# Optimization experiments

Hardware: AMD Instinct MI355X
Metric: run time of the kernel (lower is better)

Reference implementation:

```python
import jax, jax.numpy as jnp
import numpy as np

L_MODES = 64
GRID = 128
OUT_GRID = 128
CIN = 64
COUT = 64
T_DIM = 256


def legendre_table(L, theta):
    """Fully-normalized associated Legendre P_bar_l^m(cos(theta)), Condon-Shortley.
    Returns (L, 2L-1, n_theta) with m indexed -(L-1)..(L-1) at axis 1."""
    nt = theta.shape[0]
    x = np.cos(theta)
    s = np.sin(theta)
    P = np.zeros((L, L, nt))
    P[0, 0] = np.sqrt(1.0 / (4.0 * np.pi))
    for m in range(1, L):
        P[m, m] = -np.sqrt((2.0 * m + 1.0) / (2.0 * m)) * s * P[m - 1, m - 1]
    for m in range(L - 1):
        P[m + 1, m] = np.sqrt(2.0 * m + 3.0) * x * P[m, m]
    for m in range(L):
        for l in range(m + 2, L):
            a = np.sqrt((4.0 * l * l - 1.0) / (l * l - m * m))
            b = np.sqrt(((l - 1.0) ** 2 - m * m) / (4.0 * (l - 1.0) ** 2 - 1.0))
            P[l, m] = a * (x * P[l - 1, m] - b * P[l - 2, m])
    T = np.zeros((L, 2 * L - 1, nt))
    for m in range(L):
        T[:, L - 1 + m, :] = P[:, m, :]
        if m > 0:
            T[:, L - 1 - m, :] = ((-1.0) ** m) * P[:, m, :]
    return T.astype(np.float32)


def setup_inputs() -> dict:
    key = jax.random.key(0)
    ks = jax.random.split(key, 8)
    theta = np.pi * (np.arange(GRID) + 0.5) / GRID
    theta_out = np.pi * (np.arange(OUT_GRID) + 0.5) / OUT_GRID
    P_in = jnp.asarray(legendre_table(L_MODES, theta))            # (L, 2L-1, GRID)
    P_out = jnp.asarray(legendre_table(L_MODES, theta_out))       # (L, 2L-1, OUT_GRID)
    quad_w = jnp.asarray((np.pi / GRID) * np.sin(theta), dtype=jnp.float32)
    scale_w = 1.0 / (CIN + COUT)
    return {
        "x": jax.random.normal(ks[0], (GRID, GRID, CIN), jnp.float32),
        "t_emb": jax.random.normal(ks[1], (T_DIM,), jnp.float32),
        "wr": scale_w * jax.random.normal(ks[2], (L_MODES, 2 * L_MODES - 1, CIN, COUT), jnp.float32),
        "wi": scale_w * jax.random.normal(ks[3], (L_MODES, 2 * L_MODES - 1, CIN, COUT), jnp.float32),
        "conv_w": jax.random.normal(ks[4], (CIN, COUT), jnp.float32) / np.sqrt(CIN),
        "conv_b": jnp.zeros((COUT,), jnp.float32),
        "time_w": jax.random.normal(ks[5], (COUT, COUT), jnp.float32),
        "dense_w": jax.random.normal(ks[6], (T_DIM, 2 * COUT), jnp.float32) / np.sqrt(T_DIM),
        "ln_scale": jnp.ones((COUT,), jnp.float32),
        "ln_bias": jnp.zeros((COUT,), jnp.float32),
        "P_in": P_in,
        "P_out": P_out,
        "quad_w": quad_w,
    }


def reference(x, t_emb, wr, wi, conv_w, conv_b, time_w, dense_w, ln_scale, ln_bias, P_in, P_out, quad_w):
    L = P_in.shape[0]
    G_out = P_out.shape[2]
    nlon = x.shape[1]
    m_idx = np.arange(-(L - 1), L)

    # ---- forward spherical harmonic transform (lon FFT + Legendre quadrature) ----
    f = jnp.fft.fft(x.astype(jnp.complex64), axis=1) * (2.0 * np.pi / nlon)  # (nlat, nlon, Cin)
    fm = f[:, np.mod(m_idx, nlon), :] * quad_w[:, None, None]                # (nlat, 2L-1, Cin)
    flm = jnp.einsum('tmc,lmt->lmc', fm, P_in)                                # (L, 2L-1, Cin)

    # ---- per-(l,m) complex spectral conv ----
    w = wr + 1j * wi
    flm = jnp.einsum('lmi,lmio->lmo', flm, w)                                 # (L, 2L-1, Cout)

    # ---- inverse SHT onto output grid ----
    g = jnp.einsum('lmo,lmt->tmo', flm, P_out)                                # (G_out, 2L-1, Cout)
    phi = 2.0 * np.pi * np.arange(G_out) / G_out
    E = jnp.asarray(np.exp(1j * np.outer(m_idx, phi)).astype(np.complex64))   # (2L-1, G_out)
    x_spec = jnp.real(jnp.einsum('tmo,mk->tko', g, E))                        # (G_out, G_out, Cout)

    # ---- residual time-conditioned path (TimeConv2D, einsum as written in source) ----
    h = jnp.einsum('lmk,ko->lmo', x, conv_w) + conv_b                          # 1x1 conv
    psi = t_emb @ dense_w
    w_t, b_t = jnp.split(psi, 2, axis=-1)
    h = jnp.einsum('ij,j,lmk->lmi', time_w, w_t, h) + b_t[None, None, :]
    h = jax.image.resize(h, (G_out, G_out, h.shape[-1]), method='bicubic')

    # ---- add, layernorm over channels, relu ----
    out = x_spec + h
    mu = jnp.mean(out, axis=-1, keepdims=True)
    var = jnp.var(out, axis=-1, keepdims=True)
    out = (out - mu) * jax.lax.rsqrt(var + 1e-6) * ln_scale + ln_bias
    return jax.nn.relu(out)
```

## Files before the change

kernel.cpp:

```cpp
#include <hip/hip_runtime.h>
#include <math.h>

#define LM 64
#define MM 127
#define GG 128
#define CC 64
#define OO 64

#define TWO_PI 6.28318530717958647692f

__global__ __launch_bounds__(256) void k_dft(const float* __restrict__ x,
                                             const float* __restrict__ quad_w,
                                             const float* __restrict__ conv_w,
                                             const float* __restrict__ conv_b,
                                             const float* __restrict__ t_emb,
                                             const float* __restrict__ dense_w,
                                             const float* __restrict__ time_w,
                                             float2* __restrict__ F,
                                             float* __restrict__ Sv,
                                             float* __restrict__ aux) {
    int b = blockIdx.x;
    int tx = threadIdx.x;

    if (b == 256) {
        __shared__ float psis[128];
        if (tx < 128) {
            float acc = 0.f;
            for (int tq = 0; tq < 256; ++tq) acc += t_emb[tq] * dense_w[tq * 128 + tx];
            psis[tx] = acc;
            aux[tx] = acc;
        }
        __syncthreads();
        if (tx < 64) {
            float tv = 0.f;
            for (int q = 0; q < 64; ++q) tv += time_w[tx * 64 + q] * psis[q];
            aux[128 + tx] = tv;
        }
        return;
    }

    int t = b >> 1, ch = b & 1;
    int c0base = ch * 32;

    __shared__ __align__(16) float xs[GG * 32];
    __shared__ float2 tab[GG];
    __shared__ float cwsl[32];
    __shared__ float Sp[2][GG];
    __shared__ float bsum_s;

    {
        const float* xp = x + (size_t)t * GG * CC + c0base;
        for (int idx = tx; idx < GG * 32 / 4; idx += 256) {
            int n = idx >> 3, cq = idx & 7;
            *(float4*)&xs[n * 32 + cq * 4] = *(const float4*)&xp[n * CC + cq * 4];
        }
    }
    if (tx < GG) {
        float ang = (TWO_PI / GG) * tx;
        tab[tx] = make_float2(cosf(ang), sinf(ang));
    }
    if (tx >= 128 && tx < 160) {
        int c = c0base + (tx - 128);
        float s = 0.f;
        for (int o = 0; o < OO; ++o) s += conv_w[c * OO + o];
        cwsl[tx - 128] = s;
    }
    if (tx == 160) {
        float bs = 0.f;
        for (int o = 0; o < OO; ++o) bs += conv_b[o];
        bsum_s = bs;
    }
    __syncthreads();

    int k = tx & 63, cgl = tx >> 6;
    int c0 = cgl * 8;

    float sr[8], si[8];
#pragma unroll
    for (int j = 0; j < 8; ++j) { sr[j] = 0.f; si[j] = 0.f; }

    int kn = 0;
    for (int n = 0; n < GG; ++n) {
        float2 w = tab[kn];
        const float4 v0 = *(const float4*)&xs[n * 32 + c0];
        const float4 v1 = *(const float4*)&xs[n * 32 + c0 + 4];
        float vv[8] = {v0.x, v0.y, v0.z, v0.w, v1.x, v1.y, v1.z, v1.w};
#pragma unroll
        for (int j = 0; j < 8; ++j) {
            sr[j] += vv[j] * w.x;
            si[j] -= vv[j] * w.y;
        }
        kn = (kn + k) & (GG - 1);
    }
    float sc = (TWO_PI / GG) * quad_w[t];

    {
        float2* Fp = F + ((size_t)t * 64 + k) * CC + c0base + c0;
#pragma unroll
        for (int q = 0; q < 4; ++q) {
            float4 v = make_float4(sr[2 * q] * sc, si[2 * q] * sc,
                                   sr[2 * q + 1] * sc, si[2 * q + 1] * sc);
            *(float4*)&Fp[2 * q] = v;
        }
    }

    {
        int n2 = tx & 127, h = tx >> 7;
        float p = 0.f;
#pragma unroll
        for (int j = 0; j < 16; ++j) p += xs[n2 * 32 + h * 16 + j] * cwsl[h * 16 + j];
        Sp[h][n2] = p;
    }
    __syncthreads();
    if (tx < GG) {
        float v = Sp[0][tx] + Sp[1][tx] + (ch == 0 ? bsum_s : 0.f);
        Sv[(size_t)ch * GG * GG + t * GG + tx] = v;
    }
}

__global__ __launch_bounds__(256) void k_leg_fwd(const float2* __restrict__ F,
                                                 const float* __restrict__ P_in,
                                                 float2* __restrict__ flm) {
    int m = blockIdx.x;
    int lh = blockIdx.y;
    int l0 = lh * 32;
    if (l0 + 31 < m) return;

    __shared__ __align__(16) float2 Fs[64 * 64];
    __shared__ __align__(16) float  Ps[128 * 36];
    int tx = threadIdx.x;
    int c = tx & 63, lg = tx >> 6;

    for (int idx = tx; idx < 32 * 128; idx += 256) {
        int lr = idx >> 7, t = idx & 127;
        Ps[t * 36 + lr] = P_in[((size_t)(l0 + lr) * MM + 63 + m) * GG + t];
    }

    float sr[8], si[8];
#pragma unroll
    for (int j = 0; j < 8; ++j) { sr[j] = 0.f; si[j] = 0.f; }

    for (int tp = 0; tp < 2; ++tp) {
        __syncthreads();
        for (int idx = tx; idx < 64 * 64; idx += 256) {
            int tl = idx >> 6, cc = idx & 63;
            Fs[idx] = F[((size_t)(tp * 64 + tl) * 64 + m) * CC + cc];
        }
        __syncthreads();
        for (int tl = 0; tl < 64; ++tl) {
            int t = tp * 64 + tl;
            float2 f = Fs[tl * 64 + c];
            const float* pp = &Ps[t * 36 + lg * 8];
            float4 p0 = *(const float4*)pp;
            float4 p1 = *(const float4*)(pp + 4);
            float pv[8] = {p0.x, p0.y, p0.z, p0.w, p1.x, p1.y, p1.z, p1.w};
#pragma unroll
            for (int j = 0; j < 8; ++j) {
                sr[j] += f.x * pv[j];
                si[j] += f.y * pv[j];
            }
        }
    }
#pragma unroll
    for (int j = 0; j < 8; ++j) {
        int l = l0 + lg * 8 + j;
        if (l >= m) flm[((size_t)l * 64 + m) * CC + c] = make_float2(sr[j], si[j]);
    }
}

__global__ __launch_bounds__(256) void k_wmul(const float2* __restrict__ flm,
                                              const float* __restrict__ wr,
                                              const float* __restrict__ wi,
                                              float2* __restrict__ flm2) {
    int l = blockIdx.x, mi = blockIdx.y;
    int m = mi - 63;
    int am = m < 0 ? -m : m;
    if (l < am) return;
    __shared__ float2 fs[CC];
    __shared__ float2 part[16][CC];
    int tx = threadIdx.x, ol = tx & 15, ig = tx >> 4;
    if (tx < 64) {
        float2 f = flm[((size_t)l * 64 + am) * CC + tx];
        if (m < 0) {
            float sgn = (am & 1) ? -1.f : 1.f;
            f.x *= sgn;
            f.y *= -sgn;
        }
        fs[tx] = f;
    }
    __syncthreads();
    size_t base = ((size_t)(l * MM + mi) * CC) * OO;
    const float4* wr4 = (const float4*)(wr + base);
    const float4* wi4 = (const float4*)(wi + base);
    float ar[4] = {0.f, 0.f, 0.f, 0.f}, ai[4] = {0.f, 0.f, 0.f, 0.f};
#pragma unroll
    for (int di = 0; di < 4; ++di) {
        int i = ig * 4 + di;
        float4 a = wr4[i * 16 + ol];
        float4 b = wi4[i * 16 + ol];
        float2 f = fs[i];
        ar[0] += f.x * a.x - f.y * b.x;  ai[0] += f.x * b.x + f.y * a.x;
        ar[1] += f.x * a.y - f.y * b.y;  ai[1] += f.x * b.y + f.y * a.y;
        ar[2] += f.x * a.z - f.y * b.z;  ai[2] += f.x * b.z + f.y * a.z;
        ar[3] += f.x * a.w - f.y * b.w;  ai[3] += f.x * b.w + f.y * a.w;
    }
#pragma unroll
    for (int j = 0; j < 4; ++j) part[ig][ol * 4 + j] = make_float2(ar[j], ai[j]);
    __syncthreads();
    if (tx < 64) {
        float rr = 0.f, ri = 0.f;
#pragma unroll
        for (int q = 0; q < 16; ++q) {
            float2 p = part[q][tx];
            rr += p.x;
            ri += p.y;
        }
        flm2[(size_t)(l * MM + mi) * OO + tx] = make_float2(rr, ri);
    }
}

__global__ __launch_bounds__(256) void k_leg_inv(const float2* __restrict__ flm2,
                                                 const float* __restrict__ P_out,
                                                 float2* __restrict__ g) {
    int mi = blockIdx.x;
    int th = blockIdx.y >> 1, oh = blockIdx.y & 1;
    int t0 = th * 64, o0 = oh * 32;

    __shared__ __align__(16) float2 Ws[64 * 32];
    __shared__ __align__(16) float  Ps[64 * 64];
    int tx = threadIdx.x;
    int ol = tx & 31, tg = tx >> 5;
    int o = o0 + ol;

    for (int idx = tx; idx < 64 * 32; idx += 256) {
        int ls = idx >> 5, oo = idx & 31;
        Ws[idx] = flm2[(size_t)(ls * MM + mi) * OO + o0 + oo];
    }
    for (int idx = tx; idx < 64 * 64; idx += 256) {
        int ls = idx >> 6, tt = idx & 63;
        Ps[idx] = P_out[((size_t)ls * MM + mi) * GG + t0 + tt];
    }
    __syncthreads();

    float gr[8], gi[8];
#pragma unroll
    for (int j = 0; j < 8; ++j) { gr[j] = 0.f; gi[j] = 0.f; }

    for (int l = 0; l < 64; ++l) {
        float2 wv = Ws[l * 32 + ol];
        const float* pp = &Ps[l * 64 + tg * 8];
        float4 p0 = *(const float4*)pp;
        float4 p1 = *(const float4*)(pp + 4);
        float pv[8] = {p0.x, p0.y, p0.z, p0.w, p1.x, p1.y, p1.z, p1.w};
#pragma unroll
        for (int j = 0; j < 8; ++j) {
            gr[j] += wv.x * pv[j];
            gi[j] += wv.y * pv[j];
        }
    }
#pragma unroll
    for (int j = 0; j < 8; ++j) {
        int t = t0 + tg * 8 + j;
        g[((size_t)t * MM + mi) * OO + o] = make_float2(gr[j], gi[j]);
    }
}

__global__ __launch_bounds__(512) void k_final(const float2* __restrict__ g,
                                               const float* __restrict__ Sv,
                                               const float* __restrict__ aux,
                                               const float* __restrict__ ln_scale,
                                               const float* __restrict__ ln_bias,
                                               float* __restrict__ out) {
    __shared__ float2 gs[64 * 64];
    __shared__ float Ss[64];
    int t = blockIdx.x, kh = blockIdx.y;
    int tx = threadIdx.x;
    int o = tx & 63, kg = tx >> 6;

    if (tx < 64)
        Ss[tx] = Sv[t * GG + kh * 64 + tx] + Sv[GG * GG + t * GG + kh * 64 + tx];

    float zr[8], zi[8], accr[8], acci[8];
#pragma unroll
    for (int j = 0; j < 8; ++j) {
        int k = kh * 64 + kg * 8 + j;
        float phi = (TWO_PI / GG) * k;
        float s, c;
        __sincosf(phi, &s, &c);
        zr[j] = c; zi[j] = s;
        accr[j] = 0.f; acci[j] = 0.f;
    }

    for (int pass = 0; pass < 2; ++pass) {
        int mbase = (pass == 0) ? 64 : 0;
        int cnt = (pass == 0) ? 63 : 64;
        __syncthreads();
        for (int idx = tx; idx < cnt * 64; idx += 512) {
            int mm = idx >> 6, oo = idx & 63;
            gs[idx] = g[((size_t)t * MM + mbase + mm) * OO + oo];
        }
        __syncthreads();
        for (int mm = cnt - 1; mm >= 0; --mm) {
            float2 gv = gs[mm * 64 + o];
#pragma unroll
            for (int j = 0; j < 8; ++j) {
                float tr = accr[j] * zr[j] - acci[j] * zi[j] + gv.x;
                float ti = accr[j] * zi[j] + acci[j] * zr[j] + gv.y;
                accr[j] = tr; acci[j] = ti;
            }
        }
    }

    float tvec = aux[128 + o], bt = aux[64 + o];
    float lns = ln_scale[o], lnb = ln_bias[o];
#pragma unroll
    for (int j = 0; j < 8; ++j) {
        int k = kh * 64 + kg * 8 + j;
        float phi = (TWO_PI / GG) * k;
        float s63, c63;
        sincosf(63.f * phi, &s63, &c63);
        float xsp = accr[j] * c63 + acci[j] * s63;
        float val = xsp + tvec * Ss[k - kh * 64] + bt;

        float mu = val;
#pragma unroll
        for (int off = 1; off < 64; off <<= 1) mu += __shfl_xor(mu, off);
        mu *= (1.f / 64.f);
        float d = val - mu;
        float var = d * d;
#pragma unroll
        for (int off = 1; off < 64; off <<= 1) var += __shfl_xor(var, off);
        var *= (1.f / 64.f);
        float r = d * rsqrtf(var + 1e-6f) * lns + lnb;
        out[((size_t)(t * GG) + k) * OO + o] = fmaxf(r, 0.f);
    }
}

extern "C" void kernel_launch(void* const* d_in, const int* in_sizes, int n_in,
                              void* d_out, int out_size, void* d_ws, size_t ws_size,
                              hipStream_t stream) {
    const float* x        = (const float*)d_in[0];
    const float* t_emb    = (const float*)d_in[1];
    const float* wr       = (const float*)d_in[2];
    const float* wi       = (const float*)d_in[3];
    const float* conv_w   = (const float*)d_in[4];
    const float* conv_b   = (const float*)d_in[5];
    const float* time_w   = (const float*)d_in[6];
    const float* dense_w  = (const float*)d_in[7];
    const float* ln_scale = (const float*)d_in[8];
    const float* ln_bias  = (const float*)d_in[9];
    const float* P_in     = (const float*)d_in[10];
    const float* P_out    = (const float*)d_in[11];
    const float* quad_w   = (const float*)d_in[12];

    float* ws = (float*)d_ws;
    float*  aux  = ws;
    float2* F    = (float2*)(ws + 512);
    float2* flm  = (float2*)(ws + 1049088);
    float2* flm2 = (float2*)(ws + 1573376);
    float2* g    = (float2*)(ws + 2613760);
    float*  Sv   = ws + 4694528;

    float* out = (float*)d_out;

    k_dft<<<257, 256, 0, stream>>>(x, quad_w, conv_w, conv_b, t_emb, dense_w, time_w,
                                   F, Sv, aux);
    k_leg_fwd<<<dim3(64, 2), 256, 0, stream>>>(F, P_in, flm);
    k_wmul<<<dim3(LM, MM), 256, 0, stream>>>(flm, wr, wi, flm2);
    k_leg_inv<<<dim3(MM, 4), 256, 0, stream>>>(flm2, P_out, g);
    k_final<<<dim3(GG, 2), 512, 0, stream>>>(g, Sv, aux, ln_scale, ln_bias, out);
}
```

Measured before the change: 341.5 us.

## Split DFT, forward Legendre and inverse Legendre across more blocks for occupancy

The channel-split DFT now runs 512 blocks of 16 channels, and the forward Legendre transform is split over four theta chunks that write partial sums which k_wmul reduces. The inverse Legendre kernel uses smaller theta tiles, giving twice as many blocks. k_final replaces a per-element sincosf(63*phi) with a sign-flip identity and sums four partial S vectors. The aim is to fill more compute units on small grids, at the cost of extra partial-sum traffic and less per-thread reuse.

```diff
diff --git a/kernel.cpp b/kernel.cpp
--- a/kernel.cpp
+++ b/kernel.cpp
@@ -22,7 +22,7 @@
     int b = blockIdx.x;
     int tx = threadIdx.x;
 
-    if (b == 256) {
+    if (b == 512) {
         __shared__ float psis[128];
         if (tx < 128) {
             float acc = 0.f;
@@ -39,54 +39,54 @@
         return;
     }
 
-    int t = b >> 1, ch = b & 1;
-    int c0base = ch * 32;
-
-    __shared__ __align__(16) float xs[GG * 32];
+    int t = b >> 2, cq = b & 3;
+    int c0base = cq * 16;
+
+    __shared__ __align__(16) float xs[GG * 16];
     __shared__ float2 tab[GG];
-    __shared__ float cwsl[32];
+    __shared__ float cwsl[16];
     __shared__ float Sp[2][GG];
     __shared__ float bsum_s;
 
     {
         const float* xp = x + (size_t)t * GG * CC + c0base;
-        for (int idx = tx; idx < GG * 32 / 4; idx += 256) {
-            int n = idx >> 3, cq = idx & 7;
-            *(float4*)&xs[n * 32 + cq * 4] = *(const float4*)&xp[n * CC + cq * 4];
+        for (int idx = tx; idx < GG * 16 / 4; idx += 256) {
+            int n = idx >> 2, c4 = idx & 3;
+            *(float4*)&xs[n * 16 + c4 * 4] = *(const float4*)&xp[n * CC + c4 * 4];
         }
     }
     if (tx < GG) {
         float ang = (TWO_PI / GG) * tx;
         tab[tx] = make_float2(cosf(ang), sinf(ang));
     }
-    if (tx >= 128 && tx < 160) {
+    if (tx >= 128 && tx < 144) {
         int c = c0base + (tx - 128);
         float s = 0.f;
         for (int o = 0; o < OO; ++o) s += conv_w[c * OO + o];
         cwsl[tx - 128] = s;
     }
-    if (tx == 160) {
+    if (tx == 144) {
         float bs = 0.f;
         for (int o = 0; o < OO; ++o) bs += conv_b[o];
         bsum_s = bs;
     }
     __syncthreads();
 
-    int k = tx & 63, cgl = tx >> 6;
-    int c0 = cgl * 8;
-
-    float sr[8], si[8];
-#pragma unroll
-    for (int j = 0; j < 8; ++j) { sr[j] = 0.f; si[j] = 0.f; }
+    int k = tx & 63, cg = tx >> 6;
+    int c0 = cg * 4;
+
+    float sr[4], si[4];
+#pragma unroll
+    for (int j = 0; j < 4; ++j) { sr[j] = 0.f; si[j] = 0.f; }
 
     int kn = 0;
+#pragma unroll 4
     for (int n = 0; n < GG; ++n) {
         float2 w = tab[kn];
-        const float4 v0 = *(const float4*)&xs[n * 32 + c0];
-        const float4 v1 = *(const float4*)&xs[n * 32 + c0 + 4];
-        float vv[8] = {v0.x, v0.y, v0.z, v0.w, v1.x, v1.y, v1.z, v1.w};
-#pragma unroll
-        for (int j = 0; j < 8; ++j) {
+        const float4 v = *(const float4*)&xs[n * 16 + c0];
+        float vv[4] = {v.x, v.y, v.z, v.w};
+#pragma unroll
+        for (int j = 0; j < 4; ++j) {
             sr[j] += vv[j] * w.x;
             si[j] -= vv[j] * w.y;
         }
@@ -96,79 +96,75 @@
 
     {
         float2* Fp = F + ((size_t)t * 64 + k) * CC + c0base + c0;
-#pragma unroll
-        for (int q = 0; q < 4; ++q) {
-            float4 v = make_float4(sr[2 * q] * sc, si[2 * q] * sc,
-                                   sr[2 * q + 1] * sc, si[2 * q + 1] * sc);
-            *(float4*)&Fp[2 * q] = v;
-        }
+        *(float4*)&Fp[0] = make_float4(sr[0] * sc, si[0] * sc, sr[1] * sc, si[1] * sc);
+        *(float4*)&Fp[2] = make_float4(sr[2] * sc, si[2] * sc, sr[3] * sc, si[3] * sc);
     }
 
     {
         int n2 = tx & 127, h = tx >> 7;
         float p = 0.f;
 #pragma unroll
-        for (int j = 0; j < 16; ++j) p += xs[n2 * 32 + h * 16 + j] * cwsl[h * 16 + j];
+        for (int j = 0; j < 8; ++j) p += xs[n2 * 16 + h * 8 + j] * cwsl[h * 8 + j];
         Sp[h][n2] = p;
     }
     __syncthreads();
     if (tx < GG) {
-        float v = Sp[0][tx] + Sp[1][tx] + (ch == 0 ? bsum_s : 0.f);
-        Sv[(size_t)ch * GG * GG + t * GG + tx] = v;
+        float v = Sp[0][tx] + Sp[1][tx] + (cq == 0 ? bsum_s : 0.f);
+        Sv[(size_t)cq * GG * GG + t * GG + tx] = v;
     }
 }
 
 __global__ __launch_bounds__(256) void k_leg_fwd(const float2* __restrict__ F,
                                                  const float* __restrict__ P_in,
-                                                 float2* __restrict__ flm) {
+                                                 float2* __restrict__ flmp) {
     int m = blockIdx.x;
     int lh = blockIdx.y;
+    int tq = blockIdx.z;
     int l0 = lh * 32;
     if (l0 + 31 < m) return;
-
-    __shared__ __align__(16) float2 Fs[64 * 64];
-    __shared__ __align__(16) float  Ps[128 * 36];
+    int t0 = tq * 32;
+
+    __shared__ __align__(16) float2 Fs[32 * 64];
+    __shared__ __align__(16) float  Ps[32 * 36];
     int tx = threadIdx.x;
     int c = tx & 63, lg = tx >> 6;
 
-    for (int idx = tx; idx < 32 * 128; idx += 256) {
-        int lr = idx >> 7, t = idx & 127;
-        Ps[t * 36 + lr] = P_in[((size_t)(l0 + lr) * MM + 63 + m) * GG + t];
-    }
+    for (int idx = tx; idx < 32 * 32; idx += 256) {
+        int lr = idx >> 5, tl = idx & 31;
+        Ps[tl * 36 + lr] = P_in[((size_t)(l0 + lr) * MM + 63 + m) * GG + t0 + tl];
+    }
+    for (int idx = tx; idx < 32 * 64; idx += 256) {
+        int tl = idx >> 6, cc = idx & 63;
+        Fs[idx] = F[((size_t)(t0 + tl) * 64 + m) * CC + cc];
+    }
+    __syncthreads();
 
     float sr[8], si[8];
 #pragma unroll
     for (int j = 0; j < 8; ++j) { sr[j] = 0.f; si[j] = 0.f; }
 
-    for (int tp = 0; tp < 2; ++tp) {
-        __syncthreads();
-        for (int idx = tx; idx < 64 * 64; idx += 256) {
-            int tl = idx >> 6, cc = idx & 63;
-            Fs[idx] = F[((size_t)(tp * 64 + tl) * 64 + m) * CC + cc];
-        }
-        __syncthreads();
-        for (int tl = 0; tl < 64; ++tl) {
-            int t = tp * 64 + tl;
-            float2 f = Fs[tl * 64 + c];
-            const float* pp = &Ps[t * 36 + lg * 8];
-            float4 p0 = *(const float4*)pp;
-            float4 p1 = *(const float4*)(pp + 4);
-            float pv[8] = {p0.x, p0.y, p0.z, p0.w, p1.x, p1.y, p1.z, p1.w};
-#pragma unroll
-            for (int j = 0; j < 8; ++j) {
-                sr[j] += f.x * pv[j];
-                si[j] += f.y * pv[j];
-            }
+#pragma unroll 2
+    for (int tl = 0; tl < 32; ++tl) {
+        float2 f = Fs[tl * 64 + c];
+        const float* pp = &Ps[tl * 36 + lg * 8];
+        float4 p0 = *(const float4*)pp;
+        float4 p1 = *(const float4*)(pp + 4);
+        float pv[8] = {p0.x, p0.y, p0.z, p0.w, p1.x, p1.y, p1.z, p1.w};
+#pragma unroll
+        for (int j = 0; j < 8; ++j) {
+            sr[j] += f.x * pv[j];
+            si[j] += f.y * pv[j];
         }
     }
 #pragma unroll
     for (int j = 0; j < 8; ++j) {
         int l = l0 + lg * 8 + j;
-        if (l >= m) flm[((size_t)l * 64 + m) * CC + c] = make_float2(sr[j], si[j]);
-    }
-}
-
-__global__ __launch_bounds__(256) void k_wmul(const float2* __restrict__ flm,
+        if (l >= m)
+            flmp[(((size_t)tq * 64 + l) * 64 + m) * CC + c] = make_float2(sr[j], si[j]);
+    }
+}
+
+__global__ __launch_bounds__(256) void k_wmul(const float2* __restrict__ flmp,
                                               const float* __restrict__ wr,
                                               const float* __restrict__ wi,
                                               float2* __restrict__ flm2) {
@@ -180,7 +176,13 @@
     __shared__ float2 part[16][CC];
     int tx = threadIdx.x, ol = tx & 15, ig = tx >> 4;
     if (tx < 64) {
-        float2 f = flm[((size_t)l * 64 + am) * CC + tx];
+        float2 f = make_float2(0.f, 0.f);
+#pragma unroll
+        for (int q = 0; q < 4; ++q) {
+            float2 v = flmp[(((size_t)q * 64 + l) * 64 + am) * CC + tx];
+            f.x += v.x;
+            f.y += v.y;
+        }
         if (m < 0) {
             float sgn = (am & 1) ? -1.f : 1.f;
             f.x *= sgn;
@@ -224,10 +226,10 @@
                                                  float2* __restrict__ g) {
     int mi = blockIdx.x;
     int th = blockIdx.y >> 1, oh = blockIdx.y & 1;
-    int t0 = th * 64, o0 = oh * 32;
+    int t0 = th * 32, o0 = oh * 32;
 
     __shared__ __align__(16) float2 Ws[64 * 32];
-    __shared__ __align__(16) float  Ps[64 * 64];
+    __shared__ __align__(16) float  Ps[64 * 32];
     int tx = threadIdx.x;
     int ol = tx & 31, tg = tx >> 5;
     int o = o0 + ol;
@@ -236,31 +238,30 @@
         int ls = idx >> 5, oo = idx & 31;
         Ws[idx] = flm2[(size_t)(ls * MM + mi) * OO + o0 + oo];
     }
-    for (int idx = tx; idx < 64 * 64; idx += 256) {
-        int ls = idx >> 6, tt = idx & 63;
+    for (int idx = tx; idx < 64 * 32; idx += 256) {
+        int ls = idx >> 5, tt = idx & 31;
         Ps[idx] = P_out[((size_t)ls * MM + mi) * GG + t0 + tt];
     }
     __syncthreads();
 
-    float gr[8], gi[8];
-#pragma unroll
-    for (int j = 0; j < 8; ++j) { gr[j] = 0.f; gi[j] = 0.f; }
-
+    float gr[4], gi[4];
+#pragma unroll
+    for (int j = 0; j < 4; ++j) { gr[j] = 0.f; gi[j] = 0.f; }
+
+#pragma unroll 2
     for (int l = 0; l < 64; ++l) {
         float2 wv = Ws[l * 32 + ol];
-        const float* pp = &Ps[l * 64 + tg * 8];
-        float4 p0 = *(const float4*)pp;
-        float4 p1 = *(const float4*)(pp + 4);
-        float pv[8] = {p0.x, p0.y, p0.z, p0.w, p1.x, p1.y, p1.z, p1.w};
-#pragma unroll
-        for (int j = 0; j < 8; ++j) {
+        const float4 p = *(const float4*)&Ps[l * 32 + tg * 4];
+        float pv[4] = {p.x, p.y, p.z, p.w};
+#pragma unroll
+        for (int j = 0; j < 4; ++j) {
             gr[j] += wv.x * pv[j];
             gi[j] += wv.y * pv[j];
         }
     }
 #pragma unroll
-    for (int j = 0; j < 8; ++j) {
-        int t = t0 + tg * 8 + j;
+    for (int j = 0; j < 4; ++j) {
+        int t = t0 + tg * 4 + j;
         g[((size_t)t * MM + mi) * OO + o] = make_float2(gr[j], gi[j]);
     }
 }
@@ -277,8 +278,12 @@
     int tx = threadIdx.x;
     int o = tx & 63, kg = tx >> 6;
 
-    if (tx < 64)
-        Ss[tx] = Sv[t * GG + kh * 64 + tx] + Sv[GG * GG + t * GG + kh * 64 + tx];
+    if (tx < 64) {
+        float s = 0.f;
+#pragma unroll
+        for (int q = 0; q < 4; ++q) s += Sv[(size_t)q * GG * GG + t * GG + kh * 64 + tx];
+        Ss[tx] = s;
+    }
 
     float zr[8], zi[8], accr[8], acci[8];
 #pragma unroll
@@ -286,7 +291,7 @@
         int k = kh * 64 + kg * 8 + j;
         float phi = (TWO_PI / GG) * k;
         float s, c;
-        __sincosf(phi, &s, &c);
+        sincosf(phi, &s, &c);
         zr[j] = c; zi[j] = s;
         accr[j] = 0.f; acci[j] = 0.f;
     }
@@ -316,10 +321,8 @@
 #pragma unroll
     for (int j = 0; j < 8; ++j) {
         int k = kh * 64 + kg * 8 + j;
-        float phi = (TWO_PI / GG) * k;
-        float s63, c63;
-        sincosf(63.f * phi, &s63, &c63);
-        float xsp = accr[j] * c63 + acci[j] * s63;
+        float sgn = (k & 1) ? -1.f : 1.f;
+        float xsp = sgn * (accr[j] * zr[j] - acci[j] * zi[j]);
         float val = xsp + tvec * Ss[k - kh * 64] + bt;
 
         float mu = val;
@@ -356,17 +359,17 @@
     float* ws = (float*)d_ws;
     float*  aux  = ws;
     float2* F    = (float2*)(ws + 512);
-    float2* flm  = (float2*)(ws + 1049088);
-    float2* flm2 = (float2*)(ws + 1573376);
-    float2* g    = (float2*)(ws + 2613760);
-    float*  Sv   = ws + 4694528;
+    float2* flmp = (float2*)(ws + 1049088);
+    float2* flm2 = (float2*)(ws + 3146240);
+    float2* g    = (float2*)(ws + 4186624);
+    float*  Sv   = ws + 6267392;
 
     float* out = (float*)d_out;
 
-    k_dft<<<257, 256, 0, stream>>>(x, quad_w, conv_w, conv_b, t_emb, dense_w, time_w,
+    k_dft<<<513, 256, 0, stream>>>(x, quad_w, conv_w, conv_b, t_emb, dense_w, time_w,
                                    F, Sv, aux);
-    k_leg_fwd<<<dim3(64, 2), 256, 0, stream>>>(F, P_in, flm);
-    k_wmul<<<dim3(LM, MM), 256, 0, stream>>>(flm, wr, wi, flm2);
-    k_leg_inv<<<dim3(MM, 4), 256, 0, stream>>>(flm2, P_out, g);
+    k_leg_fwd<<<dim3(64, 2, 4), 256, 0, stream>>>(F, P_in, flmp);
+    k_wmul<<<dim3(LM, MM), 256, 0, stream>>>(flmp, wr, wi, flm2);
+    k_leg_inv<<<dim3(MM, 8), 256, 0, stream>>>(flm2, P_out, g);
     k_final<<<dim3(GG, 2), 512, 0, stream>>>(g, Sv, aux, ln_scale, ln_bias, out);
 }
```

After: 325.5 us. 1.05x faster.
